# Kernel optimization log

Measured on AMD Instinct MI355X. Metric: run time of the kernel, lower is better.

The kernel has to match this reference:

```python
import jax, jax.numpy as jnp
import numpy as np

RADIUS = 0.2
NSAMPLE = 32
EPS = 1e-5  # BatchNorm2d default eps


def _bn_relu(x, g, b):
    # BatchNorm2d in training mode: per-channel stats over (B, S, nsample), biased var.
    m = x.mean(axis=(0, 1, 2))
    v = jnp.mean((x - m) ** 2, axis=(0, 1, 2))
    return jax.nn.relu((x - m) * jax.lax.rsqrt(v + EPS) * g + b)


def setup_inputs() -> dict:
    key = jax.random.key(0)
    ks = jax.random.split(key, 8)
    B, N, S = 8, 8192, 2048
    xyz = jax.random.uniform(ks[0], (B, 3, N), dtype=jnp.float32)          # unit cube
    points = jax.random.normal(ks[1], (B, 3, N), dtype=jnp.float32)
    fps_idx = jax.random.randint(ks[2], (B, S), 0, N, dtype=jnp.int32)
    W1 = jax.random.normal(ks[3], (64, 6), dtype=jnp.float32) * 0.1
    W2 = jax.random.normal(ks[4], (64, 64), dtype=jnp.float32) * 0.1
    W3 = jax.random.normal(ks[5], (128, 64), dtype=jnp.float32) * 0.1
    return dict(
        xyz=xyz, points=points, fps_idx=fps_idx,
        W1=W1, g1=jnp.ones((64,)), b1=jnp.zeros((64,)),
        W2=W2, g2=jnp.ones((64,)), b2=jnp.zeros((64,)),
        W3=W3, g3=jnp.ones((128,)), b3=jnp.zeros((128,)),
    )


def reference(xyz, points, fps_idx, W1, g1, b1, W2, g2, b2, W3, g3, b3):
    B, _, N = xyz.shape
    xyz_t = jnp.transpose(xyz, (0, 2, 1))            # [B,N,3]
    pts_t = jnp.transpose(points, (0, 2, 1))         # [B,N,D]
    # gather_operation: sampled centers
    new_xyz_t = jnp.take_along_axis(xyz_t, fps_idx[:, :, None], axis=1)  # [B,S,3]
    # ball query: first NSAMPLE points within radius; pad with first hit
    d2 = jnp.sum((new_xyz_t[:, :, None, :] - xyz_t[:, None, :, :]) ** 2, axis=-1)  # [B,S,N]
    keys = jnp.where(d2 <= RADIUS * RADIUS, jnp.arange(N, dtype=jnp.int32), N)
    neg_top, _ = jax.lax.top_k(-keys, NSAMPLE)       # smallest keys first
    idx = -neg_top                                   # [B,S,NSAMPLE]
    idx = jnp.where(idx < N, idx, idx[:, :, 0:1])    # pad empty slots with first hit (self always in-radius)
    bidx = jnp.arange(B)[:, None, None]
    grouped_xyz = xyz_t[bidx, idx]                   # [B,S,ns,3]
    rel = grouped_xyz - new_xyz_t[:, :, None, :]     # center-relative coords
    grouped_pts = pts_t[bidx, idx]                   # [B,S,ns,D]
    feat = jnp.concatenate([rel, grouped_pts], axis=-1)  # [B,S,ns,3+D]
    for W, g, b in ((W1, g1, b1), (W2, g2, b2), (W3, g3, b3)):
        feat = _bn_relu(jnp.einsum('bsnc,oc->bsno', feat, W), g, b)
    new_points = jnp.max(feat, axis=2)               # max over neighbors -> [B,S,C]
    return jnp.transpose(new_xyz_t, (0, 2, 1)), jnp.transpose(new_points, (0, 2, 1))
```

## Files before the change

kernel.cpp:

```cpp
#include <hip/hip_runtime.h>
#include <hip/hip_bf16.h>

#define BB_ 8
#define NN_ 8192
#define SS_ 2048
#define NS 32
#define C1 64
#define C2 64
#define C3 128
#define RAD2 0.04f
#define BN_EPS 1e-5f
#define M_TOT (BB_*SS_*NS)
#define INV_M (1.0f/524288.0f)
#define YSTR 34

typedef __attribute__((ext_vector_type(8))) short bf16x8;
typedef __attribute__((ext_vector_type(4))) float f32x4;

#define FBF_OFF 0
#define WPK_OFF 2097152
#define ST_OFF  2104320
#define GMM_OFF 2104832
#define X2_OFF  4201984
#define WS_NEED ((size_t)(4201984 + 16777216) * 4)

__device__ inline unsigned pkbf(float a, float b) {
    __hip_bfloat162 h = __float22bfloat162_rn(make_float2(a, b));
    unsigned r; __builtin_memcpy(&r, &h, 4); return r;
}
__device__ inline bf16x8 asfrag(uint4 v) { bf16x8 r; __builtin_memcpy(&r, &v, 16); return r; }
__device__ inline float bflo(unsigned u) { unsigned x = u << 16; float f; __builtin_memcpy(&f, &x, 4); return f; }
__device__ inline float bfhi(unsigned u) { unsigned x = u & 0xffff0000u; float f; __builtin_memcpy(&f, &x, 4); return f; }

__device__ inline void fin1_ch(const float* __restrict__ st, const float* __restrict__ W1,
                               const float* __restrict__ g, const float* __restrict__ bb,
                               int o, float* __restrict__ al, float* __restrict__ cl) {
    float w[6];
    #pragma unroll
    for (int i = 0; i < 6; ++i) w[i] = W1[o * 6 + i];
    float ms = 0.f;
    #pragma unroll
    for (int i = 0; i < 6; ++i) ms = fmaf(w[i], st[i], ms);
    float m = ms * INV_M;
    float e2 = 0.f;
    #pragma unroll
    for (int ci = 0; ci < 6; ++ci)
        #pragma unroll
        for (int d = 0; d < 6; ++d) {
            int lo = ci < d ? ci : d, hi = ci < d ? d : ci;
            int idx = 6 + lo * 6 - lo * (lo + 1) / 2 + hi;
            e2 = fmaf(w[ci] * w[d], st[idx], e2);
        }
    float var = e2 * INV_M - m * m;
    float ai = g[o] * (1.0f / sqrtf(var + BN_EPS));
    al[o] = ai;
    cl[o] = bb[o] - m * ai;
}

__device__ inline void fin_ch(const float* __restrict__ sum, const float* __restrict__ sq,
                              const float* __restrict__ g, const float* __restrict__ bb,
                              int o, float* __restrict__ al, float* __restrict__ cl) {
    float m = sum[o] * INV_M;
    float var = sq[o] * INV_M - m * m;
    float ai = g[o] * (1.0f / sqrtf(var + BN_EPS));
    al[o] = ai;
    cl[o] = bb[o] - m * ai;
}

__global__ void k_front(const float* __restrict__ xyz, const float* __restrict__ pts,
                        const int* __restrict__ fps, uint4* __restrict__ fbf,
                        const float* __restrict__ W1, const float* __restrict__ W2,
                        const float* __restrict__ W3, uint4* __restrict__ wf,
                        float* __restrict__ st) {
    __shared__ int lidx[4][NS];
    int tid = threadIdx.x;
    if (blockIdx.x >= 4096) {
        int bb = blockIdx.x - 4096;
        if (bb == 7) { st[tid] = 0.f; st[tid + 256] = 0.f; return; }
        int t = bb * 256 + tid;
        int l = t & 63, p = l & 15, qd = l >> 4;
        float v[8];
        if (t < 256) {
            int mt = t >> 6;
            #pragma unroll
            for (int j = 0; j < 8; ++j)
                v[j] = (qd == 0 && j < 6) ? W1[(mt * 16 + p) * 6 + j] : 0.f;
        } else if (t < 768) {
            int fr = (t - 256) >> 6;
            int mt = fr >> 1, kf = fr & 1;
            #pragma unroll
            for (int j = 0; j < 8; ++j)
                v[j] = W2[(16 * mt + p) * 64 + kf * 32 + qd * 8 + j];
        } else {
            int fr = (t - 768) >> 6;
            int nt = fr >> 1, kf = fr & 1;
            #pragma unroll
            for (int j = 0; j < 8; ++j)
                v[j] = W3[(nt * 16 + p) * 64 + kf * 32 + qd * 8 + j];
        }
        uint4 o;
        o.x = pkbf(v[0], v[1]); o.y = pkbf(v[2], v[3]);
        o.z = pkbf(v[4], v[5]); o.w = pkbf(v[6], v[7]);
        wf[t] = o;
        return;
    }
    int wave = (blockIdx.x * blockDim.x + tid) >> 6;
    int lane = tid & 63;
    int wslot = tid >> 6;
    int b = wave / SS_;
    const float* xb = xyz + (size_t)b * 3 * NN_;
    const float* pb = pts + (size_t)b * 3 * NN_;
    int ci = fps[wave];
    float cx = xb[ci], cy = xb[NN_ + ci], cz = xb[2 * NN_ + ci];

    float px = xb[lane], py = xb[NN_ + lane], pz = xb[2 * NN_ + lane];
    int found = 0;
    int first_i = -1;
    for (int base = 0; base < NN_; base += 64) {
        float xv = px, yv = py, zv = pz;
        int nb = (base + 64 < NN_) ? base + 64 : 0;
        px = xb[nb + lane]; py = xb[NN_ + nb + lane]; pz = xb[2 * NN_ + nb + lane];
        float dx = xv - cx, dy = yv - cy, dz = zv - cz;
        float d2 = __fadd_rn(__fadd_rn(__fmul_rn(dx, dx), __fmul_rn(dy, dy)), __fmul_rn(dz, dz));
        bool inr = d2 <= RAD2;
        unsigned long long mask = __ballot(inr);
        if (first_i < 0 && mask) first_i = base + __builtin_ctzll(mask);
        if (inr) {
            int pos = found + __popcll(mask & ((1ull << lane) - 1ull));
            if (pos < NS) lidx[wslot][pos] = base + lane;
        }
        found += __popcll(mask);
        if (found >= NS) break;
    }
    if (found > NS) found = NS;
    if (lane < NS) {
        int j = (lane < found) ? lidx[wslot][lane] : first_i;
        uint4 o;
        o.x = pkbf(xb[j] - cx,           xb[NN_ + j] - cy);
        o.y = pkbf(xb[2 * NN_ + j] - cz, pb[j]);
        o.z = pkbf(pb[NN_ + j],          pb[2 * NN_ + j]);
        o.w = 0u;
        fbf[(size_t)wave * NS + lane] = o;
    }
}

__global__ void k_p1(const uint4* __restrict__ fbf, float* __restrict__ st) {
    __shared__ float sacc[27];
    int tid = threadIdx.x;
    if (tid < 27) sacc[tid] = 0.f;
    __syncthreads();
    int gt = blockIdx.x * 256 + tid;
    float vals[27];
    #pragma unroll
    for (int i = 0; i < 27; ++i) vals[i] = 0.f;
    #pragma unroll 1
    for (int it = 0; it < M_TOT / 65536; ++it) {
        uint4 w = fbf[it * 65536 + gt];
        float f[6] = { bflo(w.x), bfhi(w.x), bflo(w.y), bfhi(w.y), bflo(w.z), bfhi(w.z) };
        #pragma unroll
        for (int c = 0; c < 6; ++c) vals[c] += f[c];
        int q = 6;
        #pragma unroll
        for (int c = 0; c < 6; ++c)
            #pragma unroll
            for (int d = c; d < 6; ++d) { vals[q] = fmaf(f[c], f[d], vals[q]); ++q; }
    }
    int lane = tid & 63;
    #pragma unroll
    for (int i = 0; i < 27; ++i) {
        float v = vals[i];
        #pragma unroll
        for (int d = 32; d; d >>= 1) v += __shfl_xor(v, d);
        if (lane == 0) atomicAdd(&sacc[i], v);
    }
    __syncthreads();
    if (tid < 27) atomicAdd(&st[tid], sacc[tid]);
}

__global__ __launch_bounds__(256) void k_p2(
        const uint4* __restrict__ fbf, const uint4* __restrict__ wpk,
        float* __restrict__ st,
        const float* __restrict__ W1, const float* __restrict__ g1, const float* __restrict__ b1,
        uint4* __restrict__ x2a, int store_x2) {
    __shared__ unsigned yls[4][64 * YSTR];
    __shared__ float bs[C2], bq[C2];
    __shared__ float a1ls[C1], c1ls[C1];
    int tid = threadIdx.x, wslot = tid >> 6, lane = tid & 63;
    int p = lane & 15, qd = lane >> 4;
    int tile = blockIdx.x * 4 + wslot;
    int base = tile * 64;
    uint4 bv[4];
    #pragma unroll
    for (int nt = 0; nt < 4; ++nt) {
        uint4 v = make_uint4(0u, 0u, 0u, 0u);
        if (qd == 0) v = fbf[base + nt * 16 + p];
        bv[nt] = v;
    }
    if (tid < C2) { bs[tid] = 0.f; bq[tid] = 0.f; fin1_ch(st, W1, g1, b1, tid, a1ls, c1ls); }
    __syncthreads();
    const uint4* w1f = wpk;
    const uint4* w2f = wpk + 256;
    unsigned* my = yls[wslot];
    float s2[4][4], q2[4][4];
    #pragma unroll
    for (int i = 0; i < 4; ++i)
        #pragma unroll
        for (int r = 0; r < 4; ++r) { s2[i][r] = 0.f; q2[i][r] = 0.f; }

    bf16x8 B1[4];
    #pragma unroll
    for (int nt = 0; nt < 4; ++nt) B1[nt] = asfrag(bv[nt]);
    #pragma unroll
    for (int mt = 0; mt < 4; ++mt) {
        bf16x8 A = asfrag(w1f[mt * 64 + lane]);
        float4 av = *(const float4*)(a1ls + mt * 16 + qd * 4);
        float4 cv = *(const float4*)(c1ls + mt * 16 + qd * 4);
        #pragma unroll
        for (int nt = 0; nt < 4; ++nt) {
            f32x4 acc = {0.f, 0.f, 0.f, 0.f};
            acc = __builtin_amdgcn_mfma_f32_16x16x32_bf16(A, B1[nt], acc, 0, 0, 0);
            float y0 = fmaxf(fmaf(av.x, acc[0], cv.x), 0.f);
            float y1 = fmaxf(fmaf(av.y, acc[1], cv.y), 0.f);
            float y2 = fmaxf(fmaf(av.z, acc[2], cv.z), 0.f);
            float y3 = fmaxf(fmaf(av.w, acc[3], cv.w), 0.f);
            int a = (nt * 16 + p) * YSTR + mt * 8 + qd * 2;
            *(uint2*)&my[a] = make_uint2(pkbf(y0, y1), pkbf(y2, y3));
        }
    }
    __syncthreads();
    bf16x8 B2[4][2];
    #pragma unroll
    for (int nt = 0; nt < 4; ++nt)
        #pragma unroll
        for (int kf = 0; kf < 2; ++kf)
            B2[nt][kf] = asfrag(*(const uint4*)&my[(nt * 16 + p) * YSTR + kf * 16 + qd * 4]);
    __syncthreads();
    #pragma unroll
    for (int mt = 0; mt < 4; ++mt) {
        f32x4 acc[4];
        #pragma unroll
        for (int nt = 0; nt < 4; ++nt) acc[nt] = (f32x4){0.f, 0.f, 0.f, 0.f};
        #pragma unroll
        for (int kf = 0; kf < 2; ++kf) {
            bf16x8 W = asfrag(w2f[(mt * 2 + kf) * 64 + lane]);
            #pragma unroll
            for (int nt = 0; nt < 4; ++nt)
                acc[nt] = __builtin_amdgcn_mfma_f32_16x16x32_bf16(W, B2[nt][kf], acc[nt], 0, 0, 0);
        }
        if (store_x2) {
            #pragma unroll
            for (int nt = 0; nt < 4; ++nt) {
                int a = (nt * 16 + p) * YSTR + mt * 8 + qd * 2;
                *(uint2*)&my[a] = make_uint2(pkbf(acc[nt][0], acc[nt][1]),
                                             pkbf(acc[nt][2], acc[nt][3]));
            }
        }
        #pragma unroll
        for (int r = 0; r < 4; ++r) {
            float u0 = acc[0][r], u1 = acc[1][r], u2 = acc[2][r], u3 = acc[3][r];
            s2[mt][r] += (u0 + u1) + (u2 + u3);
            q2[mt][r] = fmaf(u0, u0, fmaf(u1, u1, fmaf(u2, u2, fmaf(u3, u3, q2[mt][r]))));
        }
    }
    if (store_x2) {
        __syncthreads();
        #pragma unroll
        for (int mtc = 0; mtc < 4; ++mtc)
            #pragma unroll
            for (int kf = 0; kf < 2; ++kf) {
                uint4 v = *(const uint4*)&my[(mtc * 16 + p) * YSTR + kf * 16 + qd * 4];
                x2a[((size_t)tile * 8 + mtc * 2 + kf) * 64 + lane] = v;
            }
    }
    #pragma unroll
    for (int mt = 0; mt < 4; ++mt)
        #pragma unroll
        for (int r = 0; r < 4; ++r) {
            float s = s2[mt][r], q = q2[mt][r];
            #pragma unroll
            for (int off = 1; off <= 8; off <<= 1) { s += __shfl_xor(s, off); q += __shfl_xor(q, off); }
            if (p == 0) {
                atomicAdd(&bs[mt * 16 + qd * 4 + r], s);
                atomicAdd(&bq[mt * 16 + qd * 4 + r], q);
            }
        }
    __syncthreads();
    if (tid < C2) { atomicAdd(&st[64 + tid], bs[tid]); atomicAdd(&st[128 + tid], bq[tid]); }
}

__global__ __launch_bounds__(256) void k_p3_l3(
        const uint4* __restrict__ x2a, const uint4* __restrict__ wpk,
        float* __restrict__ st,
        const float* __restrict__ g2, const float* __restrict__ b2,
        const float* __restrict__ g3, float* __restrict__ gmm) {
    __shared__ uint4 w3ls[1024];
    __shared__ float bs[C3], bq[C3];
    __shared__ float a2ls[C2], c2ls[C2];
    int tid = threadIdx.x, wslot = tid >> 6, lane = tid & 63;
    int p = lane & 15, qd = lane >> 4;
    int tile = blockIdx.x * 4 + wslot;
    size_t cb = (size_t)tile * 8;
    uint4 cur[8];
    #pragma unroll
    for (int i = 0; i < 8; ++i) cur[i] = x2a[(cb + i) * 64 + lane];
    bool pos[8];
    #pragma unroll
    for (int i = 0; i < 8; ++i) pos[i] = g3[i * 16 + p] >= 0.f;
    if (tid < 128) bs[tid] = 0.f; else bq[tid - 128] = 0.f;
    #pragma unroll
    for (int i = 0; i < 4; ++i) w3ls[i * 256 + tid] = wpk[768 + i * 256 + tid];
    if (tid < C2) fin_ch(st + 64, st + 128, g2, b2, tid, a2ls, c2ls);
    __syncthreads();
    float a2r[2][8], c2r[2][8];
    #pragma unroll
    for (int kf = 0; kf < 2; ++kf)
        #pragma unroll
        for (int j = 0; j < 8; ++j) {
            a2r[kf][j] = a2ls[kf * 32 + qd * 8 + j];
            c2r[kf][j] = c2ls[kf * 32 + qd * 8 + j];
        }
    float gs3[8], gq3[8];
    #pragma unroll
    for (int i = 0; i < 8; ++i) { gs3[i] = 0.f; gq3[i] = 0.f; }

    bf16x8 A[4][2];
    #pragma unroll
    for (int mt = 0; mt < 4; ++mt)
        #pragma unroll
        for (int kf = 0; kf < 2; ++kf) {
            uint4 u = cur[mt * 2 + kf];
            unsigned w[4] = { u.x, u.y, u.z, u.w };
            unsigned r[4];
            #pragma unroll
            for (int wi = 0; wi < 4; ++wi) {
                float lo = bflo(w[wi]), hi = bfhi(w[wi]);
                r[wi] = pkbf(fmaxf(fmaf(a2r[kf][2 * wi], lo, c2r[kf][2 * wi]), 0.f),
                             fmaxf(fmaf(a2r[kf][2 * wi + 1], hi, c2r[kf][2 * wi + 1]), 0.f));
            }
            uint4 o = make_uint4(r[0], r[1], r[2], r[3]);
            A[mt][kf] = asfrag(o);
        }
    float va[2][8];
    #pragma unroll
    for (int nt = 0; nt < 8; ++nt) {
        bf16x8 Wa = asfrag(w3ls[(nt * 2 + 0) * 64 + lane]);
        bf16x8 Wb = asfrag(w3ls[(nt * 2 + 1) * 64 + lane]);
        #pragma unroll
        for (int mt = 0; mt < 4; ++mt) {
            f32x4 acc = __builtin_amdgcn_mfma_f32_16x16x32_bf16(A[mt][0], Wa,
                            (f32x4){0.f, 0.f, 0.f, 0.f}, 0, 0, 0);
            acc = __builtin_amdgcn_mfma_f32_16x16x32_bf16(A[mt][1], Wb, acc, 0, 0, 0);
            float v0 = acc[0], v1 = acc[1], v2 = acc[2], v3 = acc[3];
            gs3[nt] += (v0 + v1) + (v2 + v3);
            gq3[nt] = fmaf(v0, v0, fmaf(v1, v1, fmaf(v2, v2, fmaf(v3, v3, gq3[nt]))));
            float mx = fmaxf(fmaxf(v0, v1), fmaxf(v2, v3));
            float mn = fminf(fminf(v0, v1), fminf(v2, v3));
            float vv = pos[nt] ? mx : -mn;
            int g = mt >> 1;
            if ((mt & 1) == 0) va[g][nt] = vv;
            else va[g][nt] = fmaxf(va[g][nt], vv);
        }
    }
    #pragma unroll
    for (int nt = 0; nt < 8; ++nt) {
        float x = va[0][nt], y = va[1][nt];
        x = fmaxf(x, __shfl_xor(x, 16)); x = fmaxf(x, __shfl_xor(x, 32));
        y = fmaxf(y, __shfl_xor(y, 16)); y = fmaxf(y, __shfl_xor(y, 32));
        if (lane < 16) {
            gmm[(size_t)(tile * 2 + 0) * C3 + nt * 16 + lane] = x;
            gmm[(size_t)(tile * 2 + 1) * C3 + nt * 16 + lane] = y;
        }
    }
    #pragma unroll
    for (int nt = 0; nt < 8; ++nt) {
        float s = gs3[nt], q = gq3[nt];
        s += __shfl_xor(s, 16); s += __shfl_xor(s, 32);
        q += __shfl_xor(q, 16); q += __shfl_xor(q, 32);
        if (lane < 16) {
            atomicAdd(&bs[nt * 16 + lane], s);
            atomicAdd(&bq[nt * 16 + lane], q);
        }
    }
    __syncthreads();
    if (tid < C3) { atomicAdd(&st[192 + tid], bs[tid]); atomicAdd(&st[320 + tid], bq[tid]); }
}

__global__ __launch_bounds__(256) void k_p3_fused(
        const uint4* __restrict__ fbf, const uint4* __restrict__ wpk,
        float* __restrict__ st,
        const float* __restrict__ W1, const float* __restrict__ g1, const float* __restrict__ b1,
        const float* __restrict__ g2, const float* __restrict__ b2,
        const float* __restrict__ g3, float* __restrict__ gmm) {
    __shared__ unsigned yls[4][64 * YSTR];
    __shared__ uint4 w3ls[1024];
    __shared__ float bs[C3], bq[C3];
    __shared__ float a1ls[C1], c1ls[C1], a2ls[C2], c2ls[C2];
    int tid = threadIdx.x, wslot = tid >> 6, lane = tid & 63;
    int p = lane & 15, qd = lane >> 4;
    if (tid < 128) bs[tid] = 0.f; else bq[tid - 128] = 0.f;
    #pragma unroll
    for (int i = 0; i < 4; ++i) w3ls[i * 256 + tid] = wpk[768 + i * 256 + tid];
    if (tid < 64) fin1_ch(st, W1, g1, b1, tid, a1ls, c1ls);
    else if (tid < 128) fin_ch(st + 64, st + 128, g2, b2, tid - 64, a2ls, c2ls);
    __syncthreads();
    const uint4* w1f = wpk;
    const uint4* w2f = wpk + 256;
    unsigned* my = yls[wslot];
    float gs3[8], gq3[8];
    bool pos[8];
    #pragma unroll
    for (int i = 0; i < 8; ++i) { gs3[i] = 0.f; gq3[i] = 0.f; pos[i] = g3[i * 16 + p] >= 0.f; }

    #pragma unroll 1
    for (int it = 0; it < 2; ++it) {
        int tile = it * 4096 + blockIdx.x * 4 + wslot;
        int base = tile * 64;
        bf16x8 B1[4];
        #pragma unroll
        for (int nt = 0; nt < 4; ++nt) {
            uint4 v = make_uint4(0u, 0u, 0u, 0u);
            if (qd == 0) v = fbf[base + nt * 16 + p];
            B1[nt] = asfrag(v);
        }
        #pragma unroll
        for (int mt = 0; mt < 4; ++mt) {
            bf16x8 Aw = asfrag(w1f[mt * 64 + lane]);
            float4 av = *(const float4*)(a1ls + mt * 16 + qd * 4);
            float4 cv = *(const float4*)(c1ls + mt * 16 + qd * 4);
            #pragma unroll
            for (int nt = 0; nt < 4; ++nt) {
                f32x4 acc = {0.f, 0.f, 0.f, 0.f};
                acc = __builtin_amdgcn_mfma_f32_16x16x32_bf16(Aw, B1[nt], acc, 0, 0, 0);
                float y0 = fmaxf(fmaf(av.x, acc[0], cv.x), 0.f);
                float y1 = fmaxf(fmaf(av.y, acc[1], cv.y), 0.f);
                float y2 = fmaxf(fmaf(av.z, acc[2], cv.z), 0.f);
                float y3 = fmaxf(fmaf(av.w, acc[3], cv.w), 0.f);
                int a = (nt * 16 + p) * YSTR + mt * 8 + qd * 2;
                *(uint2*)&my[a] = make_uint2(pkbf(y0, y1), pkbf(y2, y3));
            }
        }
        __syncthreads();
        bf16x8 B2[4][2];
        #pragma unroll
        for (int nt = 0; nt < 4; ++nt)
            #pragma unroll
            for (int kf = 0; kf < 2; ++kf)
                B2[nt][kf] = asfrag(*(const uint4*)&my[(nt * 16 + p) * YSTR + kf * 16 + qd * 4]);
        __syncthreads();
        #pragma unroll
        for (int mt = 0; mt < 4; ++mt) {
            f32x4 acc[4];
            #pragma unroll
            for (int nt = 0; nt < 4; ++nt) acc[nt] = (f32x4){0.f, 0.f, 0.f, 0.f};
            #pragma unroll
            for (int kf = 0; kf < 2; ++kf) {
                bf16x8 W = asfrag(w2f[(mt * 2 + kf) * 64 + lane]);
                #pragma unroll
                for (int nt = 0; nt < 4; ++nt)
                    acc[nt] = __builtin_amdgcn_mfma_f32_16x16x32_bf16(W, B2[nt][kf], acc[nt], 0, 0, 0);
            }
            float4 av = *(const float4*)(a2ls + mt * 16 + qd * 4);
            float4 cv = *(const float4*)(c2ls + mt * 16 + qd * 4);
            #pragma unroll
            for (int nt = 0; nt < 4; ++nt) {
                float y0 = fmaxf(fmaf(av.x, acc[nt][0], cv.x), 0.f);
                float y1 = fmaxf(fmaf(av.y, acc[nt][1], cv.y), 0.f);
                float y2 = fmaxf(fmaf(av.z, acc[nt][2], cv.z), 0.f);
                float y3 = fmaxf(fmaf(av.w, acc[nt][3], cv.w), 0.f);
                int a = (nt * 16 + p) * YSTR + mt * 8 + qd * 2;
                *(uint2*)&my[a] = make_uint2(pkbf(y0, y1), pkbf(y2, y3));
            }
        }
        __syncthreads();
        bf16x8 A3[4][2];
        #pragma unroll
        for (int mt = 0; mt < 4; ++mt) {
            A3[mt][0] = asfrag(*(const uint4*)&my[(mt * 16 + p) * YSTR + qd * 4]);
            A3[mt][1] = asfrag(*(const uint4*)&my[(mt * 16 + p) * YSTR + 16 + qd * 4]);
        }
        __syncthreads();
        #pragma unroll
        for (int nt = 0; nt < 8; ++nt) {
            bf16x8 Wa = asfrag(w3ls[(nt * 2 + 0) * 64 + lane]);
            bf16x8 Wb = asfrag(w3ls[(nt * 2 + 1) * 64 + lane]);
            f32x4 acc[4];
            #pragma unroll
            for (int mt = 0; mt < 4; ++mt) {
                acc[mt] = __builtin_amdgcn_mfma_f32_16x16x32_bf16(A3[mt][0], Wa,
                            (f32x4){0.f, 0.f, 0.f, 0.f}, 0, 0, 0);
                acc[mt] = __builtin_amdgcn_mfma_f32_16x16x32_bf16(A3[mt][1], Wb, acc[mt], 0, 0, 0);
            }
            float s = 0.f, q = 0.f, va = 0.f, vb = 0.f;
            #pragma unroll
            for (int mt = 0; mt < 4; ++mt) {
                float v0 = acc[mt][0], v1 = acc[mt][1], v2 = acc[mt][2], v3 = acc[mt][3];
                s += (v0 + v1) + (v2 + v3);
                q = fmaf(v0, v0, fmaf(v1, v1, fmaf(v2, v2, fmaf(v3, v3, q))));
                float mx = fmaxf(fmaxf(v0, v1), fmaxf(v2, v3));
                float mn = fminf(fminf(v0, v1), fminf(v2, v3));
                float vv = pos[nt] ? mx : -mn;
                if (mt == 0) va = vv;
                else if (mt == 1) va = fmaxf(va, vv);
                else if (mt == 2) vb = vv;
                else vb = fmaxf(vb, vv);
            }
            gs3[nt] += s; gq3[nt] += q;
            va = fmaxf(va, __shfl_xor(va, 16)); va = fmaxf(va, __shfl_xor(va, 32));
            vb = fmaxf(vb, __shfl_xor(vb, 16)); vb = fmaxf(vb, __shfl_xor(vb, 32));
            if (lane < 16) {
                gmm[(size_t)(tile * 2 + 0) * C3 + nt * 16 + lane] = va;
                gmm[(size_t)(tile * 2 + 1) * C3 + nt * 16 + lane] = vb;
            }
        }
    }
    #pragma unroll
    for (int nt = 0; nt < 8; ++nt) {
        float s = gs3[nt], q = gq3[nt];
        s += __shfl_xor(s, 16); s += __shfl_xor(s, 32);
        q += __shfl_xor(q, 16); q += __shfl_xor(q, 32);
        if (lane < 16) {
            atomicAdd(&bs[nt * 16 + lane], s);
            atomicAdd(&bq[nt * 16 + lane], q);
        }
    }
    __syncthreads();
    if (tid < C3) { atomicAdd(&st[192 + tid], bs[tid]); atomicAdd(&st[320 + tid], bq[tid]); }
}

__global__ void k_outx(const float* __restrict__ gmm, const float* __restrict__ st,
                       const float* __restrict__ g3, const float* __restrict__ b3,
                       const float* __restrict__ xyz, const int* __restrict__ fps,
                       float* __restrict__ out) {
    __shared__ float T[C3][17];
    __shared__ float a3ls[C3], c3ls[C3];
    int blk = blockIdx.x, tid = threadIdx.x;
    if (blk < 1024) {
        if (tid < C3) fin_ch(st + 192, st + 320, g3, b3, tid, a3ls, c3ls);
        __syncthreads();
        int b = blk >> 7, s0 = (blk & 127) << 4;
        #pragma unroll
        for (int i = 0; i < 8; ++i) {
            int idx = i * 256 + tid;
            int sl = idx >> 7, o = idx & 127;
            float m = gmm[((size_t)(b * SS_ + s0 + sl)) * C3 + o];
            float a = a3ls[o];
            float v = (a >= 0.f) ? m : -m;
            T[o][sl] = fmaxf(fmaf(a, v, c3ls[o]), 0.f);
        }
        __syncthreads();
        int o = tid & 127, sh = tid >> 7;
        float* dst = out + (size_t)BB_ * 3 * SS_ + ((size_t)b * C3 + o) * SS_ + s0 + sh * 8;
        float4 w0, w1;
        w0.x = T[o][sh * 8 + 0]; w0.y = T[o][sh * 8 + 1];
        w0.z = T[o][sh * 8 + 2]; w0.w = T[o][sh * 8 + 3];
        w1.x = T[o][sh * 8 + 4]; w1.y = T[o][sh * 8 + 5];
        w1.z = T[o][sh * 8 + 6]; w1.w = T[o][sh * 8 + 7];
        *(float4*)dst = w0; *(float4*)(dst + 4) = w1;
    } else {
        int t = (blk - 1024) * 256 + tid;
        int b = t / (3 * SS_);
        int r = (t / SS_) % 3;
        int s = t % SS_;
        int ci = fps[b * SS_ + s];
        out[t] = xyz[((size_t)b * 3 + r) * NN_ + ci];
    }
}

extern "C" void kernel_launch(void* const* d_in, const int* in_sizes, int n_in,
                              void* d_out, int out_size, void* d_ws, size_t ws_size,
                              hipStream_t stream) {
    (void)in_sizes; (void)n_in; (void)out_size;
    const float* xyz = (const float*)d_in[0];
    const float* pts = (const float*)d_in[1];
    const int*   fps = (const int*)d_in[2];
    const float* W1 = (const float*)d_in[3];
    const float* g1 = (const float*)d_in[4];
    const float* b1 = (const float*)d_in[5];
    const float* W2 = (const float*)d_in[6];
    const float* g2 = (const float*)d_in[7];
    const float* b2 = (const float*)d_in[8];
    const float* W3 = (const float*)d_in[9];
    const float* g3 = (const float*)d_in[10];
    const float* b3 = (const float*)d_in[11];
    float* out = (float*)d_out;
    float* ws = (float*)d_ws;

    uint4* fbf = (uint4*)(ws + FBF_OFF);
    uint4* wpk = (uint4*)(ws + WPK_OFF);
    float* st  = ws + ST_OFF;
    float* gmm = ws + GMM_OFF;
    uint4* x2a = (uint4*)(ws + X2_OFF);
    int split = (ws_size >= WS_NEED) ? 1 : 0;

    k_front<<<4096 + 8, 256, 0, stream>>>(xyz, pts, fps, fbf, W1, W2, W3, wpk, st);
    k_p1<<<256, 256, 0, stream>>>(fbf, st);
    k_p2<<<2048, 256, 0, stream>>>(fbf, wpk, st, W1, g1, b1, x2a, split);
    if (split)
        k_p3_l3<<<2048, 256, 0, stream>>>(x2a, wpk, st, g2, b2, g3, gmm);
    else
        k_p3_fused<<<1024, 256, 0, stream>>>(fbf, wpk, st, W1, g1, b1, g2, b2, g3, gmm);
    k_outx<<<1024 + 192, 256, 0, stream>>>(gmm, st, g3, b3, xyz, fps, out);
}
```

Baseline: 272.1 us.

## Process two tiles per wave in p2/p3 with register prefetch of next tile

k_p2 and k_p3_l3 now have each wave handle two 64-row tiles, so the grids shrink from 2048 to 1024 blocks. The second tile's input is loaded into registers while the first is computed. W1 fragments are hoisted into registers, and the intra-wave LDS __syncthreads are replaced by compiler memory barriers because each wave owns its LDS slot. Launch-bound occupancy hints are added, which adds register pressure and halves the block count, at some risk to latency hiding.

```diff
diff --git a/kernel.cpp b/kernel.cpp
--- a/kernel.cpp
+++ b/kernel.cpp
@@ -177,7 +177,7 @@
     if (tid < 27) atomicAdd(&st[tid], sacc[tid]);
 }
 
-__global__ __launch_bounds__(256) void k_p2(
+__global__ __launch_bounds__(256, 4) void k_p2(
         const uint4* __restrict__ fbf, const uint4* __restrict__ wpk,
         float* __restrict__ st,
         const float* __restrict__ W1, const float* __restrict__ g1, const float* __restrict__ b1,
@@ -187,18 +187,19 @@
     __shared__ float a1ls[C1], c1ls[C1];
     int tid = threadIdx.x, wslot = tid >> 6, lane = tid & 63;
     int p = lane & 15, qd = lane >> 4;
-    int tile = blockIdx.x * 4 + wslot;
-    int base = tile * 64;
+    int tile0 = blockIdx.x * 8 + wslot;
     uint4 bv[4];
     #pragma unroll
     for (int nt = 0; nt < 4; ++nt) {
         uint4 v = make_uint4(0u, 0u, 0u, 0u);
-        if (qd == 0) v = fbf[base + nt * 16 + p];
+        if (qd == 0) v = fbf[tile0 * 64 + nt * 16 + p];
         bv[nt] = v;
     }
+    bf16x8 w1r[4];
+    #pragma unroll
+    for (int mt = 0; mt < 4; ++mt) w1r[mt] = asfrag(wpk[mt * 64 + lane]);
     if (tid < C2) { bs[tid] = 0.f; bq[tid] = 0.f; fin1_ch(st, W1, g1, b1, tid, a1ls, c1ls); }
     __syncthreads();
-    const uint4* w1f = wpk;
     const uint4* w2f = wpk + 256;
     unsigned* my = yls[wslot];
     float s2[4][4], q2[4][4];
@@ -207,70 +208,88 @@
         #pragma unroll
         for (int r = 0; r < 4; ++r) { s2[i][r] = 0.f; q2[i][r] = 0.f; }
 
-    bf16x8 B1[4];
-    #pragma unroll
-    for (int nt = 0; nt < 4; ++nt) B1[nt] = asfrag(bv[nt]);
-    #pragma unroll
-    for (int mt = 0; mt < 4; ++mt) {
-        bf16x8 A = asfrag(w1f[mt * 64 + lane]);
-        float4 av = *(const float4*)(a1ls + mt * 16 + qd * 4);
-        float4 cv = *(const float4*)(c1ls + mt * 16 + qd * 4);
-        #pragma unroll
-        for (int nt = 0; nt < 4; ++nt) {
-            f32x4 acc = {0.f, 0.f, 0.f, 0.f};
-            acc = __builtin_amdgcn_mfma_f32_16x16x32_bf16(A, B1[nt], acc, 0, 0, 0);
-            float y0 = fmaxf(fmaf(av.x, acc[0], cv.x), 0.f);
-            float y1 = fmaxf(fmaf(av.y, acc[1], cv.y), 0.f);
-            float y2 = fmaxf(fmaf(av.z, acc[2], cv.z), 0.f);
-            float y3 = fmaxf(fmaf(av.w, acc[3], cv.w), 0.f);
-            int a = (nt * 16 + p) * YSTR + mt * 8 + qd * 2;
-            *(uint2*)&my[a] = make_uint2(pkbf(y0, y1), pkbf(y2, y3));
-        }
-    }
-    __syncthreads();
-    bf16x8 B2[4][2];
-    #pragma unroll
-    for (int nt = 0; nt < 4; ++nt)
-        #pragma unroll
-        for (int kf = 0; kf < 2; ++kf)
-            B2[nt][kf] = asfrag(*(const uint4*)&my[(nt * 16 + p) * YSTR + kf * 16 + qd * 4]);
-    __syncthreads();
-    #pragma unroll
-    for (int mt = 0; mt < 4; ++mt) {
-        f32x4 acc[4];
-        #pragma unroll
-        for (int nt = 0; nt < 4; ++nt) acc[nt] = (f32x4){0.f, 0.f, 0.f, 0.f};
-        #pragma unroll
-        for (int kf = 0; kf < 2; ++kf) {
-            bf16x8 W = asfrag(w2f[(mt * 2 + kf) * 64 + lane]);
-            #pragma unroll
-            for (int nt = 0; nt < 4; ++nt)
-                acc[nt] = __builtin_amdgcn_mfma_f32_16x16x32_bf16(W, B2[nt][kf], acc[nt], 0, 0, 0);
+    #pragma unroll
+    for (int t = 0; t < 2; ++t) {
+        int tile = tile0 + t * 4;
+        uint4 nbv[4];
+        if (t == 0) {
+            #pragma unroll
+            for (int nt = 0; nt < 4; ++nt) {
+                uint4 v = make_uint4(0u, 0u, 0u, 0u);
+                if (qd == 0) v = fbf[(tile0 + 4) * 64 + nt * 16 + p];
+                nbv[nt] = v;
+            }
+        }
+        bf16x8 B1[4];
+        #pragma unroll
+        for (int nt = 0; nt < 4; ++nt) B1[nt] = asfrag(bv[nt]);
+        #pragma unroll
+        for (int mt = 0; mt < 4; ++mt) {
+            bf16x8 A = w1r[mt];
+            float4 av = *(const float4*)(a1ls + mt * 16 + qd * 4);
+            float4 cv = *(const float4*)(c1ls + mt * 16 + qd * 4);
+            #pragma unroll
+            for (int nt = 0; nt < 4; ++nt) {
+                f32x4 acc = {0.f, 0.f, 0.f, 0.f};
+                acc = __builtin_amdgcn_mfma_f32_16x16x32_bf16(A, B1[nt], acc, 0, 0, 0);
+                float y0 = fmaxf(fmaf(av.x, acc[0], cv.x), 0.f);
+                float y1 = fmaxf(fmaf(av.y, acc[1], cv.y), 0.f);
+                float y2 = fmaxf(fmaf(av.z, acc[2], cv.z), 0.f);
+                float y3 = fmaxf(fmaf(av.w, acc[3], cv.w), 0.f);
+                int a = (nt * 16 + p) * YSTR + mt * 8 + qd * 2;
+                *(uint2*)&my[a] = make_uint2(pkbf(y0, y1), pkbf(y2, y3));
+            }
+        }
+        asm volatile("" ::: "memory");
+        bf16x8 B2[4][2];
+        #pragma unroll
+        for (int nt = 0; nt < 4; ++nt)
+            #pragma unroll
+            for (int kf = 0; kf < 2; ++kf)
+                B2[nt][kf] = asfrag(*(const uint4*)&my[(nt * 16 + p) * YSTR + kf * 16 + qd * 4]);
+        asm volatile("" ::: "memory");
+        #pragma unroll
+        for (int mt = 0; mt < 4; ++mt) {
+            f32x4 acc[4];
+            #pragma unroll
+            for (int nt = 0; nt < 4; ++nt) acc[nt] = (f32x4){0.f, 0.f, 0.f, 0.f};
+            #pragma unroll
+            for (int kf = 0; kf < 2; ++kf) {
+                bf16x8 W = asfrag(w2f[(mt * 2 + kf) * 64 + lane]);
+                #pragma unroll
+                for (int nt = 0; nt < 4; ++nt)
+                    acc[nt] = __builtin_amdgcn_mfma_f32_16x16x32_bf16(W, B2[nt][kf], acc[nt], 0, 0, 0);
+            }
+            if (store_x2) {
+                #pragma unroll
+                for (int nt = 0; nt < 4; ++nt) {
+                    int a = (nt * 16 + p) * YSTR + mt * 8 + qd * 2;
+                    *(uint2*)&my[a] = make_uint2(pkbf(acc[nt][0], acc[nt][1]),
+                                                 pkbf(acc[nt][2], acc[nt][3]));
+                }
+            }
+            #pragma unroll
+            for (int r = 0; r < 4; ++r) {
+                float u0 = acc[0][r], u1 = acc[1][r], u2 = acc[2][r], u3 = acc[3][r];
+                s2[mt][r] += (u0 + u1) + (u2 + u3);
+                q2[mt][r] = fmaf(u0, u0, fmaf(u1, u1, fmaf(u2, u2, fmaf(u3, u3, q2[mt][r]))));
+            }
         }
         if (store_x2) {
-            #pragma unroll
-            for (int nt = 0; nt < 4; ++nt) {
-                int a = (nt * 16 + p) * YSTR + mt * 8 + qd * 2;
-                *(uint2*)&my[a] = make_uint2(pkbf(acc[nt][0], acc[nt][1]),
-                                             pkbf(acc[nt][2], acc[nt][3]));
-            }
-        }
-        #pragma unroll
-        for (int r = 0; r < 4; ++r) {
-            float u0 = acc[0][r], u1 = acc[1][r], u2 = acc[2][r], u3 = acc[3][r];
-            s2[mt][r] += (u0 + u1) + (u2 + u3);
-            q2[mt][r] = fmaf(u0, u0, fmaf(u1, u1, fmaf(u2, u2, fmaf(u3, u3, q2[mt][r]))));
-        }
-    }
-    if (store_x2) {
-        __syncthreads();
-        #pragma unroll
-        for (int mtc = 0; mtc < 4; ++mtc)
-            #pragma unroll
-            for (int kf = 0; kf < 2; ++kf) {
-                uint4 v = *(const uint4*)&my[(mtc * 16 + p) * YSTR + kf * 16 + qd * 4];
-                x2a[((size_t)tile * 8 + mtc * 2 + kf) * 64 + lane] = v;
-            }
+            asm volatile("" ::: "memory");
+            #pragma unroll
+            for (int mtc = 0; mtc < 4; ++mtc)
+                #pragma unroll
+                for (int kf = 0; kf < 2; ++kf) {
+                    uint4 v = *(const uint4*)&my[(mtc * 16 + p) * YSTR + kf * 16 + qd * 4];
+                    x2a[((size_t)tile * 8 + mtc * 2 + kf) * 64 + lane] = v;
+                }
+        }
+        if (t == 0) {
+            #pragma unroll
+            for (int nt = 0; nt < 4; ++nt) bv[nt] = nbv[nt];
+        }
+        asm volatile("" ::: "memory");
     }
     #pragma unroll
     for (int mt = 0; mt < 4; ++mt)
@@ -288,7 +307,7 @@
     if (tid < C2) { atomicAdd(&st[64 + tid], bs[tid]); atomicAdd(&st[128 + tid], bq[tid]); }
 }
 
-__global__ __launch_bounds__(256) void k_p3_l3(
+__global__ __launch_bounds__(256, 3) void k_p3_l3(
         const uint4* __restrict__ x2a, const uint4* __restrict__ wpk,
         float* __restrict__ st,
         const float* __restrict__ g2, const float* __restrict__ b2,
@@ -298,11 +317,10 @@
     __shared__ float a2ls[C2], c2ls[C2];
     int tid = threadIdx.x, wslot = tid >> 6, lane = tid & 63;
     int p = lane & 15, qd = lane >> 4;
-    int tile = blockIdx.x * 4 + wslot;
-    size_t cb = (size_t)tile * 8;
+    int tile0 = blockIdx.x * 8 + wslot;
     uint4 cur[8];
     #pragma unroll
-    for (int i = 0; i < 8; ++i) cur[i] = x2a[(cb + i) * 64 + lane];
+    for (int i = 0; i < 8; ++i) cur[i] = x2a[((size_t)tile0 * 8 + i) * 64 + lane];
     bool pos[8];
     #pragma unroll
     for (int i = 0; i < 8; ++i) pos[i] = g3[i * 16 + p] >= 0.f;
@@ -323,52 +341,66 @@
     #pragma unroll
     for (int i = 0; i < 8; ++i) { gs3[i] = 0.f; gq3[i] = 0.f; }
 
-    bf16x8 A[4][2];
-    #pragma unroll
-    for (int mt = 0; mt < 4; ++mt)
-        #pragma unroll
-        for (int kf = 0; kf < 2; ++kf) {
-            uint4 u = cur[mt * 2 + kf];
-            unsigned w[4] = { u.x, u.y, u.z, u.w };
-            unsigned r[4];
-            #pragma unroll
-            for (int wi = 0; wi < 4; ++wi) {
-                float lo = bflo(w[wi]), hi = bfhi(w[wi]);
-                r[wi] = pkbf(fmaxf(fmaf(a2r[kf][2 * wi], lo, c2r[kf][2 * wi]), 0.f),
-                             fmaxf(fmaf(a2r[kf][2 * wi + 1], hi, c2r[kf][2 * wi + 1]), 0.f));
-            }
-            uint4 o = make_uint4(r[0], r[1], r[2], r[3]);
-            A[mt][kf] = asfrag(o);
-        }
-    float va[2][8];
-    #pragma unroll
-    for (int nt = 0; nt < 8; ++nt) {
-        bf16x8 Wa = asfrag(w3ls[(nt * 2 + 0) * 64 + lane]);
-        bf16x8 Wb = asfrag(w3ls[(nt * 2 + 1) * 64 + lane]);
-        #pragma unroll
-        for (int mt = 0; mt < 4; ++mt) {
-            f32x4 acc = __builtin_amdgcn_mfma_f32_16x16x32_bf16(A[mt][0], Wa,
-                            (f32x4){0.f, 0.f, 0.f, 0.f}, 0, 0, 0);
-            acc = __builtin_amdgcn_mfma_f32_16x16x32_bf16(A[mt][1], Wb, acc, 0, 0, 0);
-            float v0 = acc[0], v1 = acc[1], v2 = acc[2], v3 = acc[3];
-            gs3[nt] += (v0 + v1) + (v2 + v3);
-            gq3[nt] = fmaf(v0, v0, fmaf(v1, v1, fmaf(v2, v2, fmaf(v3, v3, gq3[nt]))));
-            float mx = fmaxf(fmaxf(v0, v1), fmaxf(v2, v3));
-            float mn = fminf(fminf(v0, v1), fminf(v2, v3));
-            float vv = pos[nt] ? mx : -mn;
-            int g = mt >> 1;
-            if ((mt & 1) == 0) va[g][nt] = vv;
-            else va[g][nt] = fmaxf(va[g][nt], vv);
-        }
-    }
-    #pragma unroll
-    for (int nt = 0; nt < 8; ++nt) {
-        float x = va[0][nt], y = va[1][nt];
-        x = fmaxf(x, __shfl_xor(x, 16)); x = fmaxf(x, __shfl_xor(x, 32));
-        y = fmaxf(y, __shfl_xor(y, 16)); y = fmaxf(y, __shfl_xor(y, 32));
-        if (lane < 16) {
-            gmm[(size_t)(tile * 2 + 0) * C3 + nt * 16 + lane] = x;
-            gmm[(size_t)(tile * 2 + 1) * C3 + nt * 16 + lane] = y;
+    #pragma unroll
+    for (int t = 0; t < 2; ++t) {
+        int tile = tile0 + t * 4;
+        uint4 nxt[8];
+        if (t == 0) {
+            #pragma unroll
+            for (int i = 0; i < 8; ++i)
+                nxt[i] = x2a[((size_t)(tile0 + 4) * 8 + i) * 64 + lane];
+        }
+        bf16x8 A[4][2];
+        #pragma unroll
+        for (int mt = 0; mt < 4; ++mt)
+            #pragma unroll
+            for (int kf = 0; kf < 2; ++kf) {
+                uint4 u = cur[mt * 2 + kf];
+                unsigned w[4] = { u.x, u.y, u.z, u.w };
+                unsigned r[4];
+                #pragma unroll
+                for (int wi = 0; wi < 4; ++wi) {
+                    float lo = bflo(w[wi]), hi = bfhi(w[wi]);
+                    r[wi] = pkbf(fmaxf(fmaf(a2r[kf][2 * wi], lo, c2r[kf][2 * wi]), 0.f),
+                                 fmaxf(fmaf(a2r[kf][2 * wi + 1], hi, c2r[kf][2 * wi + 1]), 0.f));
+                }
+                uint4 o = make_uint4(r[0], r[1], r[2], r[3]);
+                A[mt][kf] = asfrag(o);
+            }
+        float va[2][8];
+        #pragma unroll
+        for (int nt = 0; nt < 8; ++nt) {
+            bf16x8 Wa = asfrag(w3ls[(nt * 2 + 0) * 64 + lane]);
+            bf16x8 Wb = asfrag(w3ls[(nt * 2 + 1) * 64 + lane]);
+            #pragma unroll
+            for (int mt = 0; mt < 4; ++mt) {
+                f32x4 acc = __builtin_amdgcn_mfma_f32_16x16x32_bf16(A[mt][0], Wa,
+                                (f32x4){0.f, 0.f, 0.f, 0.f}, 0, 0, 0);
+                acc = __builtin_amdgcn_mfma_f32_16x16x32_bf16(A[mt][1], Wb, acc, 0, 0, 0);
+                float v0 = acc[0], v1 = acc[1], v2 = acc[2], v3 = acc[3];
+                gs3[nt] += (v0 + v1) + (v2 + v3);
+                gq3[nt] = fmaf(v0, v0, fmaf(v1, v1, fmaf(v2, v2, fmaf(v3, v3, gq3[nt]))));
+                float mx = fmaxf(fmaxf(v0, v1), fmaxf(v2, v3));
+                float mn = fminf(fminf(v0, v1), fminf(v2, v3));
+                float vv = pos[nt] ? mx : -mn;
+                int g = mt >> 1;
+                if ((mt & 1) == 0) va[g][nt] = vv;
+                else va[g][nt] = fmaxf(va[g][nt], vv);
+            }
+        }
+        #pragma unroll
+        for (int nt = 0; nt < 8; ++nt) {
+            float x = va[0][nt], y = va[1][nt];
+            x = fmaxf(x, __shfl_xor(x, 16)); x = fmaxf(x, __shfl_xor(x, 32));
+            y = fmaxf(y, __shfl_xor(y, 16)); y = fmaxf(y, __shfl_xor(y, 32));
+            if (lane < 16) {
+                gmm[(size_t)(tile * 2 + 0) * C3 + nt * 16 + lane] = x;
+                gmm[(size_t)(tile * 2 + 1) * C3 + nt * 16 + lane] = y;
+            }
+        }
+        if (t == 0) {
+            #pragma unroll
+            for (int i = 0; i < 8; ++i) cur[i] = nxt[i];
         }
     }
     #pragma unroll
@@ -594,9 +626,9 @@
 
     k_front<<<4096 + 8, 256, 0, stream>>>(xyz, pts, fps, fbf, W1, W2, W3, wpk, st);
     k_p1<<<256, 256, 0, stream>>>(fbf, st);
-    k_p2<<<2048, 256, 0, stream>>>(fbf, wpk, st, W1, g1, b1, x2a, split);
+    k_p2<<<1024, 256, 0, stream>>>(fbf, wpk, st, W1, g1, b1, x2a, split);
     if (split)
-        k_p3_l3<<<2048, 256, 0, stream>>>(x2a, wpk, st, g2, b2, g3, gmm);
+        k_p3_l3<<<1024, 256, 0, stream>>>(x2a, wpk, st, g2, b2, g3, gmm);
     else
         k_p3_fused<<<1024, 256, 0, stream>>>(fbf, wpk, st, W1, g1, b1, g2, b2, g3, gmm);
     k_outx<<<1024 + 192, 256, 0, stream>>>(gmm, st, g3, b3, xyz, fps, out);
```

Result: slower. 288.1 us (+5.9%).
